# Kernel optimization log

Hardware: AMD Instinct MI355X
Metric: run time of the kernel (lower is better)

## Reference

```python
import jax, jax.numpy as jnp
import numpy as np

PAD = 32       # F.pad(..., (32,32,32,32))
N_INST = 32    # labels in [0, 32]; one-hot drops background -> 32 instance channels
EPS = 1e-6


def _lovasz_hinge_flat(logits, labels):
    # logits, labels: [P] flattened over instances*H*W (per_image=False)
    signs = 2.0 * labels - 1.0
    errors = 1.0 - logits * signs
    order = jnp.argsort(-errors)               # descending sort of errors
    errors_sorted = errors[order]
    labels_sorted = labels[order]
    gts = jnp.sum(labels_sorted)
    inter = gts - jnp.cumsum(labels_sorted)
    union = gts + jnp.cumsum(1.0 - labels_sorted)
    jaccard = 1.0 - inter / union
    grad = jnp.concatenate([jaccard[:1], jaccard[1:] - jaccard[:-1]])
    return jnp.dot(jax.nn.relu(errors_sorted), jax.lax.stop_gradient(grad))


def _per_image_loss(emb, w, gt, W1, b1, W2, b2):
    # emb: [C,H,W], w: [1,H,W], gt: [1,H,W] int
    emb = jnp.pad(emb, ((0, 0), (PAD, PAD), (PAD, PAD)))
    w = jnp.pad(w, ((0, 0), (PAD, PAD), (PAD, PAD)))[0]      # [H',W']
    gt = jnp.pad(gt, ((0, 0), (PAD, PAD), (PAD, PAD)))[0]    # [H',W']
    # one-hot over instance ids 1..N_INST (background dropped): [N,H',W']
    oh = (gt[None, :, :] == jnp.arange(1, N_INST + 1)[:, None, None]).astype(emb.dtype)
    # weighted per-instance counts and centroids
    counts = jnp.einsum('nhw,hw->n', oh, w) + EPS                     # [N]
    centers = jnp.einsum('nhw,chw,hw->nc', oh, emb, w) / counts[:, None]  # [N,C]
    # sims = centers broadcast minus embeddings: [N,C,H',W']
    sims = centers[:, :, None, None] - emb[None]
    # per-pixel classifier MLP (flatten -> Linear -> ReLU -> Linear -> fold)
    h = jax.nn.relu(jnp.einsum('nchw,ck->nkhw', sims, W1) + b1[None, :, None, None])
    logits = jnp.einsum('nkhw,k->nhw', h, W2[:, 0]) + b2[0]           # probs[:,0]
    return _lovasz_hinge_flat(logits.reshape(-1), oh.reshape(-1))


def setup_inputs() -> dict:
    key = jax.random.key(0)
    k = jax.random.split(key, 8)
    B, C, H, Wd, HID = 4, 16, 192, 192, 32
    return {
        'y_embeddings': jax.random.normal(k[0], (B, C, H, Wd), jnp.float32),
        'y_weights': jax.random.uniform(k[1], (B, 1, H, Wd), jnp.float32),
        'y_true': jax.random.randint(k[2], (B, 1, H, Wd), 0, N_INST + 1),
        'W1': jax.random.normal(k[3], (C, HID), jnp.float32) * 0.1,
        'b1': jnp.zeros((HID,), jnp.float32),
        'W2': jax.random.normal(k[4], (HID, 1), jnp.float32) * 0.1,
        'b2': jnp.zeros((1,), jnp.float32),
    }


def reference(y_embeddings, y_weights, y_true, W1, b1, W2, b2):
    # random labels over 192^2 pixels guarantee every image has positives,
    # so the torch `if torch.any(gt>0)` branch is always taken -> plain mean.
    losses = jax.vmap(_per_image_loss, in_axes=(0, 0, 0, None, None, None, None))(
        y_embeddings, y_weights, y_true, W1, b1, W2, b2)
    return jnp.mean(losses)
```

## Files before the change

kernel.cpp:

```cpp
#include <hip/hip_runtime.h>

#define NBINS 2048
#define B 4
#define C 16
#define HID 32
#define NI 32
#define INTER 36864
#define PADMULT 28672
#define EPSF 1e-6f
#define THR 256
#define BPI 144
#define NBLK (B * BPI)

#define OFF_COUNTS 0
#define OFF_CSUMS  (OFF_COUNTS + B*NI)
#define OFF_V      (OFF_CSUMS + B*NI*C)
#define OFF_PERR   (OFF_V + B*NI*HID)
#define OFF_MKEY   (OFF_PERR + B*NI)
#define OFF_RANGE  (OFF_MKEY + B)
#define CTRL_END   (OFF_RANGE + 2*B)
#define OFF_F64    8192

__device__ inline unsigned fmap(float f) {
    unsigned u = __float_as_uint(f);
    return (u & 0x80000000u) ? ~u : (u | 0x80000000u);
}
__device__ inline float funmap(unsigned k) {
    return (k & 0x80000000u) ? __uint_as_float(k & 0x7fffffffu)
                             : __uint_as_float(~k);
}

__global__ void k_init(unsigned* wsu, float* out) {
    for (int i = threadIdx.x; i < CTRL_END; i += 256) wsu[i] = 0u;
    if (threadIdx.x == 0) out[0] = 0.f;
}

__global__ __launch_bounds__(THR, 4) void k_stats(
        const float* __restrict__ emb, const float* __restrict__ wgt,
        const int* __restrict__ gt, float* ws, unsigned* wsu) {
    __shared__ float s_cnt[NI];
    __shared__ float s_sum[NI * 17];
    __shared__ unsigned s_mk;
    int tid = threadIdx.x, bx = blockIdx.x;
    int img = bx / BPI;
    int q = (bx - img * BPI) * THR + tid;
    for (int i = tid; i < NI; i += THR) s_cnt[i] = 0.f;
    for (int i = tid; i < NI * 17; i += THR) s_sum[i] = 0.f;
    if (tid == 0) s_mk = 0u;
    __syncthreads();

    int g = gt[img * INTER + q];
    const float* ep = emb + (size_t)img * C * INTER + q;
    float e[C];
    float nrm = 0.f;
    #pragma unroll
    for (int c = 0; c < C; c++) { e[c] = ep[c * INTER]; nrm = fmaf(e[c], e[c], nrm); }
    if (g > 0) {
        float wv = wgt[img * INTER + q];
        atomicAdd(&s_cnt[g - 1], wv);
        #pragma unroll
        for (int c = 0; c < C; c++)
            atomicAdd(&s_sum[(g - 1) * 17 + c], e[c] * wv);
    }
    atomicMax(&s_mk, fmap(nrm));
    __syncthreads();
    for (int i = tid; i < NI; i += THR)
        atomicAdd(&ws[OFF_COUNTS + img * NI + i], s_cnt[i]);
    for (int i = tid; i < NI * C; i += THR) {
        int n = i / C, c = i - n * C;
        atomicAdd(&ws[OFF_CSUMS + (img * NI + n) * C + c], s_sum[n * 17 + c]);
    }
    if (tid == 0) atomicMax(&wsu[OFF_MKEY + img], s_mk);
}

__global__ void k_centers(const float* __restrict__ W1, const float* __restrict__ b1,
                          const float* __restrict__ W2, const float* __restrict__ b2,
                          float* ws, unsigned* wsu) {
    int im = blockIdx.x, tid = threadIdx.x;
    __shared__ float s_v[NI * HID];
    __shared__ float s_a[HID];
    __shared__ unsigned s_lo, s_hi;
    unsigned long long* f64 = (unsigned long long*)(wsu + OFF_F64) + (size_t)im * NBINS;
    for (int i = tid; i < NBINS; i += THR) f64[i] = 0ull;
    float b2v = b2[0];
    float M = sqrtf(funmap(wsu[OFF_MKEY + im]));
    if (tid < HID) {
        float ssq = 0.f;
        #pragma unroll
        for (int c = 0; c < C; c++)
            ssq = fmaf(W1[c * HID + tid], W1[c * HID + tid], ssq);
        s_a[tid] = M * sqrtf(ssq);
    }
    if (tid == 0) { s_lo = 0xFFFFFFFFu; s_hi = 0u; }
    for (int idx = tid; idx < NI * HID; idx += THR) {
        int n = idx >> 5, k = idx & 31;
        float cv = ws[OFF_COUNTS + im * NI + n] + EPSF;
        float acc = b1[k];
        #pragma unroll
        for (int c = 0; c < C; c++)
            acc += (ws[OFF_CSUMS + (im * NI + n) * C + c] / cv) * W1[c * HID + k];
        s_v[idx] = acc;
        ws[OFF_V + im * NI * HID + idx] = acc;
    }
    __syncthreads();
    if (tid < NI) {
        float lo = b2v, hi = b2v, lgp = b2v;
        #pragma unroll
        for (int k = 0; k < HID; k++) {
            float vk = s_v[tid * HID + k], a = s_a[k], w = W2[k];
            float thi = fmaxf(vk + a, 0.f), tlo = fmaxf(vk - a, 0.f);
            hi += w * (w > 0.f ? thi : tlo);
            lo += w * (w > 0.f ? tlo : thi);
            lgp = fmaf(fmaxf(vk, 0.f), w, lgp);
        }
        float pe = 1.f + lgp;
        ws[OFF_PERR + im * NI + tid] = pe;
        atomicMin(&s_lo, fmap(fminf(1.f - hi, 1.f + lo)));
        atomicMax(&s_hi, fmap(fmaxf(1.f - lo, 1.f + hi)));
    }
    __syncthreads();
    if (tid == 0) {
        ((float*)wsu)[OFF_RANGE + im * 2]     = funmap(s_lo);
        ((float*)wsu)[OFF_RANGE + im * 2 + 1] = funmap(s_hi);
    }
}

__global__ __launch_bounds__(THR, 4) void k_hist(
        const float* __restrict__ emb, const int* __restrict__ gt,
        const float* __restrict__ W1, const float* __restrict__ W2,
        const float* __restrict__ b2, const float* __restrict__ ws,
        unsigned* wsu) {
    __shared__ unsigned s_h[NBINS];
    int tid = threadIdx.x, bx = blockIdx.x;
    int img = bx / BPI;
    int q = (bx - img * BPI) * THR + tid;
    for (int i = tid; i < NBINS; i += THR) s_h[i] = 0u;
    float emin = ((const float*)wsu)[OFF_RANGE + img * 2];
    float emax = ((const float*)wsu)[OFF_RANGE + img * 2 + 1];
    float invbw = (float)NBINS / fmaxf(emax - emin, 1e-20f);
    float b2v = b2[0];
    const float* vimg = ws + OFF_V + img * NI * HID;
    __syncthreads();

    const float* ep = emb + (size_t)img * C * INTER + q;
    float u[HID];
    #pragma unroll
    for (int k = 0; k < HID; k++) u[k] = 0.f;
    #pragma unroll
    for (int c = 0; c < C; c++) {
        float ev = ep[c * INTER];
        #pragma unroll
        for (int k = 0; k < HID; k++) u[k] = fmaf(ev, W1[c * HID + k], u[k]);
    }
    int g = gt[img * INTER + q];
    #pragma unroll 4
    for (int n = 0; n < NI; n++) {
        const float* vn = vimg + n * HID;
        float lg0 = b2v, lg1 = 0.f, lg2 = 0.f, lg3 = 0.f;
        #pragma unroll
        for (int k = 0; k < HID; k += 4) {
            lg0 = fmaf(fmaxf(vn[k + 0] - u[k + 0], 0.f), W2[k + 0], lg0);
            lg1 = fmaf(fmaxf(vn[k + 1] - u[k + 1], 0.f), W2[k + 1], lg1);
            lg2 = fmaf(fmaxf(vn[k + 2] - u[k + 2], 0.f), W2[k + 2], lg2);
            lg3 = fmaf(fmaxf(vn[k + 3] - u[k + 3], 0.f), W2[k + 3], lg3);
        }
        float lg = (lg0 + lg1) + (lg2 + lg3);
        bool pos = (g == n + 1);
        float err = pos ? (1.f - lg) : (1.f + lg);
        int bn = (int)((emax - err) * invbw);
        bn = bn < 0 ? 0 : (bn >= NBINS ? NBINS - 1 : bn);
        atomicAdd(&s_h[bn], pos ? 0x10001u : 1u);
    }
    __syncthreads();
    unsigned long long* f64 = (unsigned long long*)(wsu + OFF_F64) + (size_t)img * NBINS;
    for (int i = tid; i < NBINS; i += THR) {
        unsigned pk = s_h[i];
        if (pk)
            atomicAdd(&f64[i], (unsigned long long)(pk & 0xFFFFu)
                             | ((unsigned long long)(pk >> 16) << 32));
    }
}

__global__ void k_loss(const float* ws, const unsigned* wsu, float* out) {
    const int T = 256, CHUNK = NBINS / T;
    int img = blockIdx.x, tid = threadIdx.x;
    __shared__ unsigned s_cnt[NBINS], s_pos[NBINS];
    __shared__ float s_sum[NBINS];
    __shared__ unsigned s_pc[T], s_pp[T];
    __shared__ double s_a[T];
    const unsigned long long* f64 =
        (const unsigned long long*)(wsu + OFF_F64) + (size_t)img * NBINS;
    float emin = ((const float*)wsu)[OFF_RANGE + img * 2];
    float emax = ((const float*)wsu)[OFF_RANGE + img * 2 + 1];
    float bw = (emax - emin) / (float)NBINS;
    float invbw = (float)NBINS / fmaxf(emax - emin, 1e-20f);
    for (int i = tid; i < NBINS; i += T) {
        unsigned long long pk = f64[i];
        unsigned cv = (unsigned)(pk & 0xFFFFFFFFu);
        s_cnt[i] = cv;
        s_pos[i] = (unsigned)(pk >> 32);
        float center = emax - ((float)i + 0.5f) * bw;
        s_sum[i] = (float)cv * fmaxf(center, 0.f);
    }
    __syncthreads();
    if (tid < NI) {
        float pe = ws[OFF_PERR + img * NI + tid];
        int bn = (int)((emax - pe) * invbw);
        bn = bn < 0 ? 0 : (bn >= NBINS ? NBINS - 1 : bn);
        atomicAdd(&s_cnt[bn], (unsigned)PADMULT);
        atomicAdd(&s_sum[bn], (float)PADMULT * fmaxf(pe, 0.f));
    }
    __syncthreads();
    unsigned ccnt = 0, cpos = 0;
    for (int j = 0; j < CHUNK; j++) {
        int bn = tid * CHUNK + j;
        ccnt += s_cnt[bn]; cpos += s_pos[bn];
    }
    s_pc[tid] = ccnt; s_pp[tid] = cpos;
    __syncthreads();
    for (int off = 1; off < T; off <<= 1) {
        unsigned ac = 0, ap = 0;
        if (tid >= off) { ac = s_pc[tid - off]; ap = s_pp[tid - off]; }
        __syncthreads();
        s_pc[tid] += ac; s_pp[tid] += ap;
        __syncthreads();
    }
    double Gd = (double)s_pp[T - 1];
    double r = (double)(s_pc[tid] - ccnt);
    double L = (double)(s_pp[tid] - cpos);
    double Jprev = 1.0 - (Gd - L) / (Gd + r - L);
    double acc = 0.0;
    for (int j = 0; j < CHUNK; j++) {
        int bn = tid * CHUNK + j;
        unsigned cv = s_cnt[bn], pv = s_pos[bn];
        if (cv) {
            r += (double)cv; L += (double)pv;
            double J = 1.0 - (Gd - L) / (Gd + r - L);
            double mean = (double)s_sum[bn] / (double)cv;
            acc += mean * (J - Jprev);
            Jprev = J;
        }
    }
    s_a[tid] = acc;
    __syncthreads();
    for (int s = T / 2; s > 0; s >>= 1) {
        if (tid < s) s_a[tid] += s_a[tid + s];
        __syncthreads();
    }
    if (tid == 0) atomicAdd(out, (float)(s_a[0] * 0.25));
}

extern "C" void kernel_launch(void* const* d_in, const int* in_sizes, int n_in,
                              void* d_out, int out_size, void* d_ws, size_t ws_size,
                              hipStream_t stream) {
    const float* emb = (const float*)d_in[0];
    const float* wgt = (const float*)d_in[1];
    const int*   gt  = (const int*)d_in[2];
    const float* W1  = (const float*)d_in[3];
    const float* b1  = (const float*)d_in[4];
    const float* W2  = (const float*)d_in[5];
    const float* b2  = (const float*)d_in[6];
    float* out = (float*)d_out;
    float* ws  = (float*)d_ws;
    unsigned* wsu = (unsigned*)d_ws;

    k_init<<<1, 256, 0, stream>>>(wsu, out);
    k_stats<<<NBLK, THR, 0, stream>>>(emb, wgt, gt, ws, wsu);
    k_centers<<<B, THR, 0, stream>>>(W1, b1, W2, b2, ws, wsu);
    k_hist<<<NBLK, THR, 0, stream>>>(emb, gt, W1, W2, b2, ws, wsu);
    k_loss<<<B, 256, 0, stream>>>(ws, wsu, out);
}
```

Baseline: 129.7 us.

## Fuse all five stages into one cooperative kernel with grid syncs

Merges init, stats, centers, histogram and loss kernels into a single cooperative launch separated by grid.sync barriers, with shared memory unioned across phases. Embeddings are loaded once and kept in registers, so the histogram stage no longer reads them from global memory a second time, and four launch gaps are removed. The trade-off is four grid-wide barriers and a requirement that all 576 blocks be co-resident, with launch bounds lowered to 3 blocks per CU and the u[] array now live alongside e[], which raises register pressure.

```diff
diff --git a/kernel.cpp b/kernel.cpp
--- a/kernel.cpp
+++ b/kernel.cpp
@@ -1,4 +1,6 @@
 #include <hip/hip_runtime.h>
+#include <hip/hip_cooperative_groups.h>
+namespace cg = cooperative_groups;
 
 #define NBINS 2048
 #define B 4
@@ -30,129 +32,126 @@
                              : __uint_as_float(~k);
 }
 
-__global__ void k_init(unsigned* wsu, float* out) {
-    for (int i = threadIdx.x; i < CTRL_END; i += 256) wsu[i] = 0u;
-    if (threadIdx.x == 0) out[0] = 0.f;
-}
-
-__global__ __launch_bounds__(THR, 4) void k_stats(
+struct SMemStats { float cnt[NI]; float sum[NI * 17]; unsigned mk; };
+struct SMemCent  { float v[NI * HID]; float a[HID]; unsigned lo, hi; };
+struct SMemLoss  { unsigned cnt[NBINS]; unsigned pos[NBINS]; float sum[NBINS];
+                   unsigned pc[THR]; unsigned pp[THR]; double a[THR]; };
+union SMemU { SMemStats st; SMemCent ct; unsigned h[NBINS]; SMemLoss ls; };
+
+__global__ __launch_bounds__(THR, 3) void k_fused(
         const float* __restrict__ emb, const float* __restrict__ wgt,
-        const int* __restrict__ gt, float* ws, unsigned* wsu) {
-    __shared__ float s_cnt[NI];
-    __shared__ float s_sum[NI * 17];
-    __shared__ unsigned s_mk;
+        const int* __restrict__ gt, const float* __restrict__ W1,
+        const float* __restrict__ b1, const float* __restrict__ W2,
+        const float* __restrict__ b2, float* ws, unsigned* wsu, float* out) {
+    cg::grid_group grid = cg::this_grid();
+    __shared__ SMemU sm;
     int tid = threadIdx.x, bx = blockIdx.x;
     int img = bx / BPI;
     int q = (bx - img * BPI) * THR + tid;
-    for (int i = tid; i < NI; i += THR) s_cnt[i] = 0.f;
-    for (int i = tid; i < NI * 17; i += THR) s_sum[i] = 0.f;
-    if (tid == 0) s_mk = 0u;
-    __syncthreads();
+    unsigned long long* f64all = (unsigned long long*)(wsu + OFF_F64);
+
+    {
+        unsigned gtid = (unsigned)bx * THR + tid;
+        for (unsigned i = gtid; i < CTRL_END; i += NBLK * THR) wsu[i] = 0u;
+        for (unsigned i = gtid; i < B * NBINS; i += NBLK * THR) f64all[i] = 0ull;
+        if (gtid == 0) out[0] = 0.f;
+    }
+    for (int i = tid; i < NI; i += THR) sm.st.cnt[i] = 0.f;
+    for (int i = tid; i < NI * 17; i += THR) sm.st.sum[i] = 0.f;
+    if (tid == 0) sm.st.mk = 0u;
 
     int g = gt[img * INTER + q];
+    float wv = wgt[img * INTER + q];
     const float* ep = emb + (size_t)img * C * INTER + q;
     float e[C];
     float nrm = 0.f;
     #pragma unroll
     for (int c = 0; c < C; c++) { e[c] = ep[c * INTER]; nrm = fmaf(e[c], e[c], nrm); }
+
+    grid.sync();
+
     if (g > 0) {
-        float wv = wgt[img * INTER + q];
-        atomicAdd(&s_cnt[g - 1], wv);
+        atomicAdd(&sm.st.cnt[g - 1], wv);
         #pragma unroll
         for (int c = 0; c < C; c++)
-            atomicAdd(&s_sum[(g - 1) * 17 + c], e[c] * wv);
-    }
-    atomicMax(&s_mk, fmap(nrm));
+            atomicAdd(&sm.st.sum[(g - 1) * 17 + c], e[c] * wv);
+    }
+    atomicMax(&sm.st.mk, fmap(nrm));
     __syncthreads();
     for (int i = tid; i < NI; i += THR)
-        atomicAdd(&ws[OFF_COUNTS + img * NI + i], s_cnt[i]);
+        atomicAdd(&ws[OFF_COUNTS + img * NI + i], sm.st.cnt[i]);
     for (int i = tid; i < NI * C; i += THR) {
         int n = i / C, c = i - n * C;
-        atomicAdd(&ws[OFF_CSUMS + (img * NI + n) * C + c], s_sum[n * 17 + c]);
-    }
-    if (tid == 0) atomicMax(&wsu[OFF_MKEY + img], s_mk);
-}
-
-__global__ void k_centers(const float* __restrict__ W1, const float* __restrict__ b1,
-                          const float* __restrict__ W2, const float* __restrict__ b2,
-                          float* ws, unsigned* wsu) {
-    int im = blockIdx.x, tid = threadIdx.x;
-    __shared__ float s_v[NI * HID];
-    __shared__ float s_a[HID];
-    __shared__ unsigned s_lo, s_hi;
-    unsigned long long* f64 = (unsigned long long*)(wsu + OFF_F64) + (size_t)im * NBINS;
-    for (int i = tid; i < NBINS; i += THR) f64[i] = 0ull;
-    float b2v = b2[0];
-    float M = sqrtf(funmap(wsu[OFF_MKEY + im]));
-    if (tid < HID) {
-        float ssq = 0.f;
-        #pragma unroll
-        for (int c = 0; c < C; c++)
-            ssq = fmaf(W1[c * HID + tid], W1[c * HID + tid], ssq);
-        s_a[tid] = M * sqrtf(ssq);
-    }
-    if (tid == 0) { s_lo = 0xFFFFFFFFu; s_hi = 0u; }
-    for (int idx = tid; idx < NI * HID; idx += THR) {
-        int n = idx >> 5, k = idx & 31;
-        float cv = ws[OFF_COUNTS + im * NI + n] + EPSF;
-        float acc = b1[k];
-        #pragma unroll
-        for (int c = 0; c < C; c++)
-            acc += (ws[OFF_CSUMS + (im * NI + n) * C + c] / cv) * W1[c * HID + k];
-        s_v[idx] = acc;
-        ws[OFF_V + im * NI * HID + idx] = acc;
-    }
-    __syncthreads();
-    if (tid < NI) {
-        float lo = b2v, hi = b2v, lgp = b2v;
-        #pragma unroll
-        for (int k = 0; k < HID; k++) {
-            float vk = s_v[tid * HID + k], a = s_a[k], w = W2[k];
-            float thi = fmaxf(vk + a, 0.f), tlo = fmaxf(vk - a, 0.f);
-            hi += w * (w > 0.f ? thi : tlo);
-            lo += w * (w > 0.f ? tlo : thi);
-            lgp = fmaf(fmaxf(vk, 0.f), w, lgp);
-        }
-        float pe = 1.f + lgp;
-        ws[OFF_PERR + im * NI + tid] = pe;
-        atomicMin(&s_lo, fmap(fminf(1.f - hi, 1.f + lo)));
-        atomicMax(&s_hi, fmap(fmaxf(1.f - lo, 1.f + hi)));
-    }
-    __syncthreads();
-    if (tid == 0) {
-        ((float*)wsu)[OFF_RANGE + im * 2]     = funmap(s_lo);
-        ((float*)wsu)[OFF_RANGE + im * 2 + 1] = funmap(s_hi);
-    }
-}
-
-__global__ __launch_bounds__(THR, 4) void k_hist(
-        const float* __restrict__ emb, const int* __restrict__ gt,
-        const float* __restrict__ W1, const float* __restrict__ W2,
-        const float* __restrict__ b2, const float* __restrict__ ws,
-        unsigned* wsu) {
-    __shared__ unsigned s_h[NBINS];
-    int tid = threadIdx.x, bx = blockIdx.x;
-    int img = bx / BPI;
-    int q = (bx - img * BPI) * THR + tid;
-    for (int i = tid; i < NBINS; i += THR) s_h[i] = 0u;
-    float emin = ((const float*)wsu)[OFF_RANGE + img * 2];
-    float emax = ((const float*)wsu)[OFF_RANGE + img * 2 + 1];
-    float invbw = (float)NBINS / fmaxf(emax - emin, 1e-20f);
-    float b2v = b2[0];
-    const float* vimg = ws + OFF_V + img * NI * HID;
-    __syncthreads();
-
-    const float* ep = emb + (size_t)img * C * INTER + q;
+        atomicAdd(&ws[OFF_CSUMS + (img * NI + n) * C + c], sm.st.sum[n * 17 + c]);
+    }
+    if (tid == 0) atomicMax(&wsu[OFF_MKEY + img], sm.st.mk);
+
     float u[HID];
     #pragma unroll
     for (int k = 0; k < HID; k++) u[k] = 0.f;
     #pragma unroll
     for (int c = 0; c < C; c++) {
-        float ev = ep[c * INTER];
+        float ev = e[c];
         #pragma unroll
         for (int k = 0; k < HID; k++) u[k] = fmaf(ev, W1[c * HID + k], u[k]);
     }
-    int g = gt[img * INTER + q];
+
+    grid.sync();
+
+    if (bx < B) {
+        int im = bx;
+        float b2v = b2[0];
+        float M = sqrtf(funmap(wsu[OFF_MKEY + im]));
+        if (tid < HID) {
+            float ssq = 0.f;
+            #pragma unroll
+            for (int c = 0; c < C; c++)
+                ssq = fmaf(W1[c * HID + tid], W1[c * HID + tid], ssq);
+            sm.ct.a[tid] = M * sqrtf(ssq);
+        }
+        if (tid == 0) { sm.ct.lo = 0xFFFFFFFFu; sm.ct.hi = 0u; }
+        for (int idx = tid; idx < NI * HID; idx += THR) {
+            int n = idx >> 5, k = idx & 31;
+            float cv = ws[OFF_COUNTS + im * NI + n] + EPSF;
+            float acc = b1[k];
+            #pragma unroll
+            for (int c = 0; c < C; c++)
+                acc += (ws[OFF_CSUMS + (im * NI + n) * C + c] / cv) * W1[c * HID + k];
+            sm.ct.v[idx] = acc;
+            ws[OFF_V + im * NI * HID + idx] = acc;
+        }
+        __syncthreads();
+        if (tid < NI) {
+            float lo = b2v, hi = b2v, lgp = b2v;
+            #pragma unroll
+            for (int k = 0; k < HID; k++) {
+                float vk = sm.ct.v[tid * HID + k], a = sm.ct.a[k], w = W2[k];
+                float thi = fmaxf(vk + a, 0.f), tlo = fmaxf(vk - a, 0.f);
+                hi += w * (w > 0.f ? thi : tlo);
+                lo += w * (w > 0.f ? tlo : thi);
+                lgp = fmaf(fmaxf(vk, 0.f), w, lgp);
+            }
+            float pe = 1.f + lgp;
+            ws[OFF_PERR + im * NI + tid] = pe;
+            atomicMin(&sm.ct.lo, fmap(fminf(1.f - hi, 1.f + lo)));
+            atomicMax(&sm.ct.hi, fmap(fmaxf(1.f - lo, 1.f + hi)));
+        }
+        __syncthreads();
+        if (tid == 0) {
+            ((float*)wsu)[OFF_RANGE + im * 2]     = funmap(sm.ct.lo);
+            ((float*)wsu)[OFF_RANGE + im * 2 + 1] = funmap(sm.ct.hi);
+        }
+    }
+
+    grid.sync();
+
+    for (int i = tid; i < NBINS; i += THR) sm.h[i] = 0u;
+    float emax = ((const float*)wsu)[OFF_RANGE + img * 2 + 1];
+    float emin = ((const float*)wsu)[OFF_RANGE + img * 2];
+    float invbw = (float)NBINS / fmaxf(emax - emin, 1e-20f);
+    float b2v = b2[0];
+    const float* vimg = ws + OFF_V + img * NI * HID;
+    __syncthreads();
     #pragma unroll 4
     for (int n = 0; n < NI; n++) {
         const float* vn = vimg + n * HID;
@@ -169,85 +168,85 @@
         float err = pos ? (1.f - lg) : (1.f + lg);
         int bn = (int)((emax - err) * invbw);
         bn = bn < 0 ? 0 : (bn >= NBINS ? NBINS - 1 : bn);
-        atomicAdd(&s_h[bn], pos ? 0x10001u : 1u);
+        atomicAdd(&sm.h[bn], pos ? 0x10001u : 1u);
     }
     __syncthreads();
-    unsigned long long* f64 = (unsigned long long*)(wsu + OFF_F64) + (size_t)img * NBINS;
-    for (int i = tid; i < NBINS; i += THR) {
-        unsigned pk = s_h[i];
-        if (pk)
-            atomicAdd(&f64[i], (unsigned long long)(pk & 0xFFFFu)
-                             | ((unsigned long long)(pk >> 16) << 32));
-    }
-}
-
-__global__ void k_loss(const float* ws, const unsigned* wsu, float* out) {
-    const int T = 256, CHUNK = NBINS / T;
-    int img = blockIdx.x, tid = threadIdx.x;
-    __shared__ unsigned s_cnt[NBINS], s_pos[NBINS];
-    __shared__ float s_sum[NBINS];
-    __shared__ unsigned s_pc[T], s_pp[T];
-    __shared__ double s_a[T];
-    const unsigned long long* f64 =
-        (const unsigned long long*)(wsu + OFF_F64) + (size_t)img * NBINS;
-    float emin = ((const float*)wsu)[OFF_RANGE + img * 2];
-    float emax = ((const float*)wsu)[OFF_RANGE + img * 2 + 1];
-    float bw = (emax - emin) / (float)NBINS;
-    float invbw = (float)NBINS / fmaxf(emax - emin, 1e-20f);
-    for (int i = tid; i < NBINS; i += T) {
-        unsigned long long pk = f64[i];
-        unsigned cv = (unsigned)(pk & 0xFFFFFFFFu);
-        s_cnt[i] = cv;
-        s_pos[i] = (unsigned)(pk >> 32);
-        float center = emax - ((float)i + 0.5f) * bw;
-        s_sum[i] = (float)cv * fmaxf(center, 0.f);
-    }
-    __syncthreads();
-    if (tid < NI) {
-        float pe = ws[OFF_PERR + img * NI + tid];
-        int bn = (int)((emax - pe) * invbw);
-        bn = bn < 0 ? 0 : (bn >= NBINS ? NBINS - 1 : bn);
-        atomicAdd(&s_cnt[bn], (unsigned)PADMULT);
-        atomicAdd(&s_sum[bn], (float)PADMULT * fmaxf(pe, 0.f));
-    }
-    __syncthreads();
-    unsigned ccnt = 0, cpos = 0;
-    for (int j = 0; j < CHUNK; j++) {
-        int bn = tid * CHUNK + j;
-        ccnt += s_cnt[bn]; cpos += s_pos[bn];
-    }
-    s_pc[tid] = ccnt; s_pp[tid] = cpos;
-    __syncthreads();
-    for (int off = 1; off < T; off <<= 1) {
-        unsigned ac = 0, ap = 0;
-        if (tid >= off) { ac = s_pc[tid - off]; ap = s_pp[tid - off]; }
-        __syncthreads();
-        s_pc[tid] += ac; s_pp[tid] += ap;
-        __syncthreads();
-    }
-    double Gd = (double)s_pp[T - 1];
-    double r = (double)(s_pc[tid] - ccnt);
-    double L = (double)(s_pp[tid] - cpos);
-    double Jprev = 1.0 - (Gd - L) / (Gd + r - L);
-    double acc = 0.0;
-    for (int j = 0; j < CHUNK; j++) {
-        int bn = tid * CHUNK + j;
-        unsigned cv = s_cnt[bn], pv = s_pos[bn];
-        if (cv) {
-            r += (double)cv; L += (double)pv;
-            double J = 1.0 - (Gd - L) / (Gd + r - L);
-            double mean = (double)s_sum[bn] / (double)cv;
-            acc += mean * (J - Jprev);
-            Jprev = J;
-        }
-    }
-    s_a[tid] = acc;
-    __syncthreads();
-    for (int s = T / 2; s > 0; s >>= 1) {
-        if (tid < s) s_a[tid] += s_a[tid + s];
-        __syncthreads();
-    }
-    if (tid == 0) atomicAdd(out, (float)(s_a[0] * 0.25));
+    {
+        unsigned long long* f64 = f64all + (size_t)img * NBINS;
+        for (int i = tid; i < NBINS; i += THR) {
+            unsigned pk = sm.h[i];
+            if (pk)
+                atomicAdd(&f64[i], (unsigned long long)(pk & 0xFFFFu)
+                                 | ((unsigned long long)(pk >> 16) << 32));
+        }
+    }
+
+    grid.sync();
+
+    if (bx >= B) return;
+    {
+        const int T = THR, CHUNK = NBINS / THR;
+        int im = bx;
+        const unsigned long long* f64 = f64all + (size_t)im * NBINS;
+        float lemin = ((const float*)wsu)[OFF_RANGE + im * 2];
+        float lemax = ((const float*)wsu)[OFF_RANGE + im * 2 + 1];
+        float bw = (lemax - lemin) / (float)NBINS;
+        float linv = (float)NBINS / fmaxf(lemax - lemin, 1e-20f);
+        for (int i = tid; i < NBINS; i += T) {
+            unsigned long long pk = f64[i];
+            unsigned cv = (unsigned)(pk & 0xFFFFFFFFu);
+            sm.ls.cnt[i] = cv;
+            sm.ls.pos[i] = (unsigned)(pk >> 32);
+            float center = lemax - ((float)i + 0.5f) * bw;
+            sm.ls.sum[i] = (float)cv * fmaxf(center, 0.f);
+        }
+        __syncthreads();
+        if (tid < NI) {
+            float pe = ws[OFF_PERR + im * NI + tid];
+            int bn = (int)((lemax - pe) * linv);
+            bn = bn < 0 ? 0 : (bn >= NBINS ? NBINS - 1 : bn);
+            atomicAdd(&sm.ls.cnt[bn], (unsigned)PADMULT);
+            atomicAdd(&sm.ls.sum[bn], (float)PADMULT * fmaxf(pe, 0.f));
+        }
+        __syncthreads();
+        unsigned ccnt = 0, cpos = 0;
+        for (int j = 0; j < CHUNK; j++) {
+            int bn = tid * CHUNK + j;
+            ccnt += sm.ls.cnt[bn]; cpos += sm.ls.pos[bn];
+        }
+        sm.ls.pc[tid] = ccnt; sm.ls.pp[tid] = cpos;
+        __syncthreads();
+        for (int off = 1; off < T; off <<= 1) {
+            unsigned ac = 0, ap = 0;
+            if (tid >= off) { ac = sm.ls.pc[tid - off]; ap = sm.ls.pp[tid - off]; }
+            __syncthreads();
+            sm.ls.pc[tid] += ac; sm.ls.pp[tid] += ap;
+            __syncthreads();
+        }
+        double Gd = (double)sm.ls.pp[T - 1];
+        double r = (double)(sm.ls.pc[tid] - ccnt);
+        double L = (double)(sm.ls.pp[tid] - cpos);
+        double Jprev = 1.0 - (Gd - L) / (Gd + r - L);
+        double acc = 0.0;
+        for (int j = 0; j < CHUNK; j++) {
+            int bn = tid * CHUNK + j;
+            unsigned cv = sm.ls.cnt[bn], pv = sm.ls.pos[bn];
+            if (cv) {
+                r += (double)cv; L += (double)pv;
+                double J = 1.0 - (Gd - L) / (Gd + r - L);
+                double mean = (double)sm.ls.sum[bn] / (double)cv;
+                acc += mean * (J - Jprev);
+                Jprev = J;
+            }
+        }
+        sm.ls.a[tid] = acc;
+        __syncthreads();
+        for (int s = T / 2; s > 0; s >>= 1) {
+            if (tid < s) sm.ls.a[tid] += sm.ls.a[tid + s];
+            __syncthreads();
+        }
+        if (tid == 0) atomicAdd(out, (float)(sm.ls.a[0] * 0.25));
+    }
 }
 
 extern "C" void kernel_launch(void* const* d_in, const int* in_sizes, int n_in,
@@ -264,9 +263,9 @@
     float* ws  = (float*)d_ws;
     unsigned* wsu = (unsigned*)d_ws;
 
-    k_init<<<1, 256, 0, stream>>>(wsu, out);
-    k_stats<<<NBLK, THR, 0, stream>>>(emb, wgt, gt, ws, wsu);
-    k_centers<<<B, THR, 0, stream>>>(W1, b1, W2, b2, ws, wsu);
-    k_hist<<<NBLK, THR, 0, stream>>>(emb, gt, W1, W2, b2, ws, wsu);
-    k_loss<<<B, 256, 0, stream>>>(ws, wsu, out);
-}
+    void* args[] = { (void*)&emb, (void*)&wgt, (void*)&gt, (void*)&W1,
+                     (void*)&b1, (void*)&W2, (void*)&b2,
+                     (void*)&ws, (void*)&wsu, (void*)&out };
+    hipLaunchCooperativeKernel((const void*)k_fused, dim3(NBLK), dim3(THR),
+                               args, 0, stream);
+}
```

Result: slower. 374.3 us (+188.6%).
